# Performance work log

Measured on AMD Instinct MI355X. Metric: run time of the kernel, lower is better.

The kernel has to match this reference:

```python
import jax, jax.numpy as jnp
import numpy as np
from jax import lax

B, C_IN, L = 512, 32, 512
E = 8
POOL = 16            # AdaptiveAvgPool1d(16)
D_IN = C_IN * L      # expert input = flattened x
D_OUT = 768          # pooler_output dim (hard-coded in module)
TAU = 1.0            # gumbel temperature
BN_EPS = 1e-5


def setup_inputs() -> dict:
    key = jax.random.key(0)
    ks = jax.random.split(key, 8)
    s = 0.02
    return {
        "x": jax.random.normal(ks[0], (B, C_IN, L), jnp.float32),
        "gumbel_u": jax.random.uniform(ks[1], (B, E), jnp.float32, 1e-6, 1.0 - 1e-6),
        "conv_w": jax.random.normal(ks[2], (64, C_IN, 3), jnp.float32) * s,
        "conv_b": jnp.zeros((64,), jnp.float32),
        "bn_gamma": jnp.ones((64 * POOL,), jnp.float32),
        "bn_beta": jnp.zeros((64 * POOL,), jnp.float32),
        "bn_mean": jnp.zeros((64 * POOL,), jnp.float32),
        "bn_var": jnp.ones((64 * POOL,), jnp.float32),
        "fc1_w": jax.random.normal(ks[3], (128, 64 * POOL), jnp.float32) * s,
        "fc1_b": jnp.zeros((128,), jnp.float32),
        "fc2_w": jax.random.normal(ks[4], (E, 128), jnp.float32) * s,
        "fc2_b": jnp.zeros((E,), jnp.float32),
        "expert_w": jax.random.normal(ks[5], (E, D_IN, D_OUT), jnp.float32) * s,
        "expert_b": jnp.zeros((E, D_OUT), jnp.float32),
    }


def _gelu(v):
    return jax.nn.gelu(v, approximate=False)  # torch nn.GELU default (erf)


def reference(x, gumbel_u, conv_w, conv_b, bn_gamma, bn_beta, bn_mean, bn_var,
              fc1_w, fc1_b, fc2_w, fc2_b, expert_w, expert_b):
    # ---- router ----
    h = lax.conv_general_dilated(x, conv_w, (1,), ((1, 1),),
                                 dimension_numbers=("NCH", "OIH", "NCH"))
    h = _gelu(h + conv_b[None, :, None])                     # [B,64,L]
    h = h.reshape(B, 64, POOL, L // POOL).mean(-1)           # adaptive avg pool -> [B,64,16]
    h = h.reshape(B, 64 * POOL)                              # flatten
    h = (h - bn_mean) * lax.rsqrt(bn_var + BN_EPS) * bn_gamma + bn_beta  # BN (eval)
    h = _gelu(h @ fc1_w.T + fc1_b)                           # dropout inactive in eval
    logits = h @ fc2_w.T + fc2_b                             # [B,E]

    # ---- soft gumbel-softmax gating (hard=False), then top-2 ----
    g = -jnp.log(-jnp.log(gumbel_u))
    routing_weights = jax.nn.softmax((logits + g) / TAU, axis=1)
    topv, topi = lax.top_k(routing_weights, 2)               # [B,2]
    w = topv / (topv.sum(axis=1, keepdims=True) + 1e-8)      # [B,2]

    # ---- dispatch/compute/combine (dense-expert stand-in: flatten + linear) ----
    xf = x.reshape(B, D_IN)
    all_out = jnp.einsum("bd,edh->beh", xf, expert_w) + expert_b[None]  # [B,E,768]
    sel = jnp.take_along_axis(all_out, topi[:, :, None], axis=1)        # [B,2,768]
    pooler_output = (sel * w[:, :, None]).sum(axis=1)                   # [B,768]
    return pooler_output
```

## Files before the change

kernel.cpp:

```cpp
#include <hip/hip_runtime.h>
#include <hip/hip_bf16.h>

#define NB 512
#define CIN 32
#define LEN 512
#define NE 8
#define NPOOL 16
#define DIN 16384
#define DOUT 768
#define HD 1024
#define F1 128

#define MT 128
#define NT 128
#define BK 32

typedef __attribute__((ext_vector_type(4))) float f32x4;
typedef __attribute__((ext_vector_type(8))) short s16x8;
typedef __attribute__((ext_vector_type(4))) unsigned int u32x4;

__device__ __forceinline__ float gelu_erf(float v) {
    return 0.5f * v * (1.0f + erff(v * 0.70710678118654752f));
}

__device__ __forceinline__ unsigned cvt_pk(float lo, float hi) {
    unsigned r;
    asm volatile("v_cvt_pk_bf16_f32 %0, %1, %2" : "=v"(r) : "v"(lo), "v"(hi));
    return r;
}

__device__ __forceinline__ unsigned short f2bf_u(float f) {
    union { float f; unsigned u; } x; x.f = f;
    unsigned r = x.u + 0x7fffu + ((x.u >> 16) & 1u);
    return (unsigned short)(r >> 16);
}

__device__ __forceinline__ void gload_lds16(const void* gptr, void* lptr) {
    __builtin_amdgcn_global_load_lds(
        (const __attribute__((address_space(1))) unsigned int*)gptr,
        (__attribute__((address_space(3))) unsigned int*)lptr,
        16, 0, 0);
}

__device__ __forceinline__ int bswz(int kr) {
    int g3 = kr >> 3;
    return (g3 & 3) | ((g3 & 1) << 2);
}

__global__ __launch_bounds__(256) void krouter_conv(
    const float* __restrict__ x, const float* __restrict__ cw, const float* __restrict__ cb,
    const float* __restrict__ bng, const float* __restrict__ bnb,
    const float* __restrict__ bnm, const float* __restrict__ bnv,
    float* __restrict__ h, int* __restrict__ cnt)
{
    __shared__ float xs[CIN * 264];
    int half = blockIdx.x;
    int b = blockIdx.y;
    int t = threadIdx.x;
    if (b == 0 && half == 0 && t < NE) cnt[t] = 0;

    int Lchunk0 = half * 64 - 1;
    const float* xb = x + (size_t)b * DIN;
    for (int idx = t; idx < CIN * 66; idx += 256) {
        int ci = idx / 66;
        int cc = idx - ci * 66;
        int gc = min(max(Lchunk0 + cc, 0), 127);
        f32x4 v = *(const f32x4*)(xb + ci * 512 + gc * 4);
        int byte = ci * 1056 + ((cc << 4) ^ (((cc >> 3) & 7) << 4));
        *(f32x4*)((char*)xs + byte) = v;
    }
    __syncthreads();

    int p  = t & 7;
    int pg = half * 8 + p;
    int cq = t >> 3;
    int co0 = cq * 2, co1 = co0 + 1;

    float sa[32], sb[32];
    #pragma unroll
    for (int i = 0; i < 32; ++i) { sa[i] = 0.f; sb[i] = 0.f; }

    for (int ci = 0; ci < CIN; ++ci) {
        float f[40];
        #pragma unroll
        for (int u = 0; u < 10; ++u) {
            int lc = p * 8 + u;
            int byte = ci * 1056 + ((lc << 4) ^ (((lc >> 3) & 7) << 4));
            f32x4 v = *(const f32x4*)((const char*)xs + byte);
            f[4*u+0] = v[0]; f[4*u+1] = v[1]; f[4*u+2] = v[2]; f[4*u+3] = v[3];
        }
        if (pg == 0)  f[3]  = 0.f;
        if (pg == 15) f[36] = 0.f;
        float wa0 = cw[co0*96 + ci*3 + 0], wa1 = cw[co0*96 + ci*3 + 1], wa2 = cw[co0*96 + ci*3 + 2];
        float wb0 = cw[co1*96 + ci*3 + 0], wb1 = cw[co1*96 + ci*3 + 1], wb2 = cw[co1*96 + ci*3 + 2];
        #pragma unroll
        for (int i = 0; i < 32; ++i) {
            sa[i] = fmaf(f[i+3], wa0, fmaf(f[i+4], wa1, fmaf(f[i+5], wa2, sa[i])));
            sb[i] = fmaf(f[i+3], wb0, fmaf(f[i+4], wb1, fmaf(f[i+5], wb2, sb[i])));
        }
    }

    float ba = cb[co0], bbv = cb[co1];
    float ma = 0.f, mb = 0.f;
    #pragma unroll
    for (int i = 0; i < 32; ++i) { ma += gelu_erf(sa[i] + ba); mb += gelu_erf(sb[i] + bbv); }
    ma *= (1.f / 32.f); mb *= (1.f / 32.f);

    int oa = co0 * NPOOL + pg, ob = co1 * NPOOL + pg;
    float ra = (ma - bnm[oa]) * rsqrtf(bnv[oa] + 1e-5f) * bng[oa] + bnb[oa];
    float rb = (mb - bnm[ob]) * rsqrtf(bnv[ob] + 1e-5f) * bng[ob] + bnb[ob];
    h[(size_t)b * HD + oa] = ra;
    h[(size_t)b * HD + ob] = rb;
}

__global__ __launch_bounds__(256) void krouter_fc(
    const float* __restrict__ h, const float* __restrict__ f1w, const float* __restrict__ f1b,
    const float* __restrict__ f2w, const float* __restrict__ f2b,
    const float* __restrict__ gu,
    int* __restrict__ top2e, float* __restrict__ top2w,
    int* __restrict__ cnt, int* __restrict__ rowlist, float* __restrict__ roww)
{
    __shared__ float hs[8 * HD];
    __shared__ float h1s[8 * F1];
    __shared__ float lg[8 * NE];

    int bb = blockIdx.x * 8;
    int t = threadIdx.x;

    const f32x4* hg = (const f32x4*)(h + (size_t)bb * HD);
    f32x4* hs4 = (f32x4*)hs;
    #pragma unroll
    for (int u = 0; u < 8; ++u) hs4[t + 256 * u] = hg[t + 256 * u];
    __syncthreads();

    int j = t & 127;
    int pr = t >> 7;
    float acc[4] = {0.f, 0.f, 0.f, 0.f};
    const f32x4* w4 = (const f32x4*)(f1w + (size_t)j * HD);
    for (int k4 = 0; k4 < 256; ++k4) {
        f32x4 w = w4[k4];
        #pragma unroll
        for (int g = 0; g < 4; ++g) {
            f32x4 hv = hs4[(pr * 4 + g) * 256 + k4];
            acc[g] += w[0]*hv[0] + w[1]*hv[1] + w[2]*hv[2] + w[3]*hv[3];
        }
    }
    float bj = f1b[j];
    #pragma unroll
    for (int g = 0; g < 4; ++g) h1s[(pr * 4 + g) * F1 + j] = gelu_erf(acc[g] + bj);
    __syncthreads();

    if (t < 64) {
        int bi = t >> 3, e = t & 7;
        float s = f2b[e];
        const float* w = f2w + e * F1;
        const float* hh = h1s + bi * F1;
        #pragma unroll 8
        for (int k = 0; k < F1; ++k) s += hh[k] * w[k];
        lg[bi * NE + e] = s;
    }
    __syncthreads();

    if (t < 8) {
        int bi = t; int b = bb + bi;
        float r[NE];
        float mx = -1e30f;
        #pragma unroll
        for (int e = 0; e < NE; ++e) {
            float g = -logf(-logf(gu[b * NE + e]));
            r[e] = lg[bi * NE + e] + g;
            mx = fmaxf(mx, r[e]);
        }
        float sum = 0.f;
        #pragma unroll
        for (int e = 0; e < NE; ++e) { r[e] = expf(r[e] - mx); sum += r[e]; }
        float inv = 1.f / sum;
        #pragma unroll
        for (int e = 0; e < NE; ++e) r[e] *= inv;
        int e0 = 0; float v0 = r[0];
        #pragma unroll
        for (int e = 1; e < NE; ++e) if (r[e] > v0) { v0 = r[e]; e0 = e; }
        int e1 = -1; float v1 = -1.f;
        #pragma unroll
        for (int e = 0; e < NE; ++e) { if (e == e0) continue; if (r[e] > v1) { v1 = r[e]; e1 = e; } }
        float den = v0 + v1 + 1e-8f;
        float w0 = v0 / den, w1 = v1 / den;
        top2e[b * 2 + 0] = e0; top2e[b * 2 + 1] = e1;
        top2w[b * 2 + 0] = w0; top2w[b * 2 + 1] = w1;
        int p0 = atomicAdd(&cnt[e0], 1);
        rowlist[e0 * NB + p0] = b * 2 + 0; roww[e0 * NB + p0] = w0;
        int p1 = atomicAdd(&cnt[e1], 1);
        rowlist[e1 * NB + p1] = b * 2 + 1; roww[e1 * NB + p1] = w1;
    }
}

__global__ __launch_bounds__(512, 2) void kgemm(
    const float* __restrict__ x, const float* __restrict__ ew,
    const int* __restrict__ cnt, const int* __restrict__ rowlist, const float* __restrict__ roww,
    unsigned short* __restrict__ ypart, int nkc, int kch)
{
    int bid = blockIdx.x;
    int mt = bid & 1;
    int rest = bid >> 1;
    int kc = rest % nkc;
    int rest2 = rest / nkc;
    int nt = rest2 % 6;
    int e  = rest2 / 6;
    int cn = cnt[e];

    __shared__ __align__(16) char As[2][MT * BK * 2];
    __shared__ __align__(16) char Bs[2][BK * NT * 4];

    int t = threadIdx.x;
    int wid = t >> 6, lane = t & 63;
    int wm = wid >> 2, wn = wid & 3;
    int g = lane >> 4;
    int NS = kch / BK;
    int k0 = kc * kch;

    int seg0 = wid * 2, seg1 = wid * 2 + 1;
    const char* gB = (const char*)ew + (size_t)e * DIN * DOUT * 4
                   + (size_t)k0 * (DOUT * 4) + nt * NT * 4;
    int kr0 = seg0 * 2 + (lane >> 5), cs0 = lane & 31;
    int kr1 = seg1 * 2 + (lane >> 5), cs1 = lane & 31;
    const char* gp0 = gB + (size_t)kr0 * (DOUT * 4) + ((cs0 ^ bswz(kr0)) << 4);
    const char* gp1 = gB + (size_t)kr1 * (DOUT * 4) + ((cs1 ^ bswz(kr1)) << 4);

    int ar = t >> 2, aq = t & 3;
    int aoff = ar * 64 + (((aq ^ (ar & 3))) << 4);

    for (int row0 = mt * MT; row0 < cn; row0 += 2 * MT) {
        int mloc = min(MT, cn - row0);
        int arc = min(ar, mloc - 1);
        int ent_a = rowlist[e * NB + row0 + arc];
        const float* axp = x + (size_t)(ent_a >> 1) * DIN + k0 + aq * 8;
        bool wact = (wm * 64 < mloc);

        f32x4 acc[4][2];
        #pragma unroll
        for (int i = 0; i < 4; ++i)
            #pragma unroll
            for (int jj = 0; jj < 2; ++jj) acc[i][jj] = (f32x4){0.f, 0.f, 0.f, 0.f};

        f32x4 a0, a1;
        const char* bp0 = gp0;
        const char* bp1 = gp1;

        auto stageB = [&](int bi) {
            gload_lds16(bp0, (char*)Bs[bi] + seg0 * 1024);
            gload_lds16(bp1, (char*)Bs[bi] + seg1 * 1024);
        };
        auto loadA = [&](int s) {
            const f32x4* p = (const f32x4*)(axp + (size_t)s * BK);
            a0 = p[0]; a1 = p[1];
        };
        auto storeA = [&](int bi) {
            u32x4 pk;
            pk[0] = cvt_pk(a0[0], a0[1]); pk[1] = cvt_pk(a0[2], a0[3]);
            pk[2] = cvt_pk(a1[0], a1[1]); pk[3] = cvt_pk(a1[2], a1[3]);
            *(u32x4*)(As[bi] + aoff) = pk;
        };

        stageB(0);
        loadA(0);
        storeA(0);
        __syncthreads();

        for (int s = 0; s < NS; ++s) {
            int buf = s & 1;
            if (s + 1 < NS) {
                bp0 += BK * DOUT * 4;  bp1 += BK * DOUT * 4;
                stageB(buf ^ 1);
                loadA(s + 1);
            }

            if (wact) {
                const char* Ab = As[buf];
                const char* Bb = Bs[buf];
                s16x8 af[4];
                #pragma unroll
                for (int mi = 0; mi < 4; ++mi) {
                    int m = wm * 64 + mi * 16 + (lane & 15);
                    af[mi] = *(const s16x8*)(Ab + m * 64 + ((g ^ (m & 3)) << 4));
                }
                #pragma unroll
                for (int ni = 0; ni < 2; ++ni) {
                    int n = wn * 32 + ni * 16 + (lane & 15);
                    int sw = bswz(g * 8);
                    int cbase = (((n >> 2) ^ sw) << 4) + ((n & 3) << 2);
                    float v[8];
                    #pragma unroll
                    for (int j = 0; j < 8; ++j)
                        v[j] = *(const float*)(Bb + (g * 8 + j) * 512 + cbase);
                    union { u32x4 u; s16x8 s; } bf;
                    bf.u[0] = cvt_pk(v[0], v[1]); bf.u[1] = cvt_pk(v[2], v[3]);
                    bf.u[2] = cvt_pk(v[4], v[5]); bf.u[3] = cvt_pk(v[6], v[7]);
                    #pragma unroll
                    for (int mi = 0; mi < 4; ++mi)
                        acc[mi][ni] = __builtin_amdgcn_mfma_f32_16x16x32_bf16(af[mi], bf.s, acc[mi][ni], 0, 0, 0);
                }
            }

            if (s + 1 < NS) storeA(buf ^ 1);
            __syncthreads();
        }

        if (wact) {
            #pragma unroll
            for (int mi = 0; mi < 4; ++mi) {
                #pragma unroll
                for (int rg = 0; rg < 4; ++rg) {
                    int m = wm * 64 + mi * 16 + g * 4 + rg;
                    if (m < mloc) {
                        int ent = rowlist[e * NB + row0 + m];
                        float wgt = roww[e * NB + row0 + m];
                        int ob = ent >> 1, slot = ent & 1;
                        unsigned short* dst = ypart + ((size_t)(slot * nkc + kc) * NB + ob) * DOUT
                                            + nt * NT + wn * 32 + (lane & 15);
                        #pragma unroll
                        for (int ni = 0; ni < 2; ++ni)
                            dst[ni * 16] = f2bf_u(acc[mi][ni][rg] * wgt);
                    }
                }
            }
        }
        __syncthreads();
    }
}

__global__ __launch_bounds__(256) void kcombine(
    const unsigned short* __restrict__ ypart,
    const int* __restrict__ top2e, const float* __restrict__ top2w,
    const float* __restrict__ eb, float* __restrict__ out, int nplanes)
{
    int b = blockIdx.y;
    int n = blockIdx.x * 256 + threadIdx.x;
    float s = 0.f;
    for (int p = 0; p < nplanes; ++p) {
        unsigned v = ypart[((size_t)p * NB + b) * DOUT + n];
        union { unsigned u; float f; } c; c.u = v << 16;
        s += c.f;
    }
    int e0 = top2e[b * 2], e1 = top2e[b * 2 + 1];
    float w0 = top2w[b * 2], w1 = top2w[b * 2 + 1];
    s += w0 * eb[e0 * DOUT + n] + w1 * eb[e1 * DOUT + n];
    out[(size_t)b * DOUT + n] = s;
}

extern "C" void kernel_launch(void* const* d_in, const int* in_sizes, int n_in,
                              void* d_out, int out_size, void* d_ws, size_t ws_size,
                              hipStream_t stream)
{
    const float* x   = (const float*)d_in[0];
    const float* gu  = (const float*)d_in[1];
    const float* cw  = (const float*)d_in[2];
    const float* cb  = (const float*)d_in[3];
    const float* bng = (const float*)d_in[4];
    const float* bnb = (const float*)d_in[5];
    const float* bnm = (const float*)d_in[6];
    const float* bnv = (const float*)d_in[7];
    const float* f1w = (const float*)d_in[8];
    const float* f1b = (const float*)d_in[9];
    const float* f2w = (const float*)d_in[10];
    const float* f2b = (const float*)d_in[11];
    const float* ew  = (const float*)d_in[12];
    const float* eb  = (const float*)d_in[13];

    int nkc = (ws_size >= (size_t)40 * 1024 * 1024) ? 16 : 8;
    int kch = DIN / nkc;

    char* ws = (char*)d_ws;
    size_t off = 0;
    float* h       = (float*)(ws + off); off += (size_t)NB * HD * 4;
    int*   top2e   = (int*)(ws + off);   off += (size_t)NB * 2 * 4;
    float* top2w   = (float*)(ws + off); off += (size_t)NB * 2 * 4;
    int*   cnt     = (int*)(ws + off);   off += 256;
    int*   rowlist = (int*)(ws + off);   off += (size_t)NE * NB * 4;
    float* roww    = (float*)(ws + off); off += (size_t)NE * NB * 4;
    unsigned short* ypart = (unsigned short*)(ws + off);
    off += (size_t)2 * nkc * NB * DOUT * 2;

    krouter_conv<<<dim3(2, NB), 256, 0, stream>>>(x, cw, cb, bng, bnb, bnm, bnv, h, cnt);
    krouter_fc<<<NB / 8, 256, 0, stream>>>(h, f1w, f1b, f2w, f2b, gu,
                                           top2e, top2w, cnt, rowlist, roww);
    kgemm<<<NE * 6 * nkc * 2, 512, 0, stream>>>(x, ew, cnt, rowlist, roww, ypart, nkc, kch);
    kcombine<<<dim3(3, NB), 256, 0, stream>>>(ypart, top2e, top2w, eb, (float*)d_out, 2 * nkc);
}
```

Measured before the change: 276.6 us.

## Retile expert GEMM to 256x96 tiles with XCD-aware block remap

Changes the expert GEMM tile from 128x128 to 256x96 so that a single workgroup covers up to 256 routed rows. Each weight tile is then streamed from HBM once per workgroup, instead of once for each of the two M-tile workgroups. It also remaps block IDs so consecutive blocks land on the same XCD, and moves the A store earlier so one barrier per stage can be dropped. The cost is fewer total workgroups, a larger LDS A buffer, more accumulators per wave, and an uneven B-staging split across waves.

```diff
diff --git a/kernel.cpp b/kernel.cpp
--- a/kernel.cpp
+++ b/kernel.cpp
@@ -11,8 +11,8 @@
 #define HD 1024
 #define F1 128
 
-#define MT 128
-#define NT 128
+#define MT 256
+#define NT 96
 #define BK 32
 
 typedef __attribute__((ext_vector_type(4))) float f32x4;
@@ -42,9 +42,12 @@
         16, 0, 0);
 }
 
-__device__ __forceinline__ int bswz(int kr) {
-    int g3 = kr >> 3;
+__device__ __forceinline__ int bswz(int k) {
+    int g3 = k >> 3;
     return (g3 & 3) | ((g3 & 1) << 2);
+}
+__device__ __forceinline__ int akey(int m) {
+    return (m & 3) ^ ((m >> 2) & 3);
 }
 
 __global__ __launch_bounds__(256) void krouter_conv(
@@ -199,13 +202,12 @@
     const int* __restrict__ cnt, const int* __restrict__ rowlist, const float* __restrict__ roww,
     unsigned short* __restrict__ ypart, int nkc, int kch)
 {
-    int bid = blockIdx.x;
-    int mt = bid & 1;
-    int rest = bid >> 1;
-    int kc = rest % nkc;
-    int rest2 = rest / nkc;
-    int nt = rest2 % 6;
-    int e  = rest2 / 6;
+    int nwg = gridDim.x;
+    int cpx = nwg >> 3;
+    int wg = (blockIdx.x & 7) * cpx + (blockIdx.x >> 3);
+    int nt = wg & 7;
+    int kc = (wg >> 3) % nkc;
+    int e  = wg / (8 * nkc);
     int cn = cnt[e];
 
     __shared__ __align__(16) char As[2][MT * BK * 2];
@@ -213,65 +215,82 @@
 
     int t = threadIdx.x;
     int wid = t >> 6, lane = t & 63;
-    int wm = wid >> 2, wn = wid & 3;
+    int wm = wid >> 1, wn = wid & 1;
     int g = lane >> 4;
     int NS = kch / BK;
     int k0 = kc * kch;
 
-    int seg0 = wid * 2, seg1 = wid * 2 + 1;
     const char* gB = (const char*)ew + (size_t)e * DIN * DOUT * 4
                    + (size_t)k0 * (DOUT * 4) + nt * NT * 4;
-    int kr0 = seg0 * 2 + (lane >> 5), cs0 = lane & 31;
-    int kr1 = seg1 * 2 + (lane >> 5), cs1 = lane & 31;
-    const char* gp0 = gB + (size_t)kr0 * (DOUT * 4) + ((cs0 ^ bswz(kr0)) << 4);
-    const char* gp1 = gB + (size_t)kr1 * (DOUT * 4) + ((cs1 ^ bswz(kr1)) << 4);
-
-    int ar = t >> 2, aq = t & 3;
-    int aoff = ar * 64 + (((aq ^ (ar & 3))) << 4);
-
-    for (int row0 = mt * MT; row0 < cn; row0 += 2 * MT) {
+    int seg0 = wid;
+    int seg1 = (wid < 4) ? (8 + wid) : -1;
+    int off0 = seg0 * 1024 + lane * 16;
+    int k_0 = off0 / 384, c_0 = (off0 - k_0 * 384) >> 4;
+    const char* gp0 = gB + (size_t)k_0 * (DOUT * 4) + ((c_0 ^ bswz(k_0)) << 4);
+    const char* gp1 = nullptr;
+    int ldsoff1 = 0;
+    if (seg1 >= 0) {
+        int off1 = seg1 * 1024 + lane * 16;
+        int k_1 = off1 / 384, c_1 = (off1 - k_1 * 384) >> 4;
+        gp1 = gB + (size_t)k_1 * (DOUT * 4) + ((c_1 ^ bswz(k_1)) << 4);
+        ldsoff1 = seg1 * 1024;
+    }
+    int ldsoff0 = seg0 * 1024;
+
+    int ar = t >> 1, ah = t & 1;
+    int arow_byte = ar * 64;
+    int ak = akey(ar);
+    int ac0 = ((2 * ah) ^ ak) << 4;
+    int ac1 = ((2 * ah + 1) ^ ak) << 4;
+
+    for (int row0 = 0; row0 < cn; row0 += MT) {
         int mloc = min(MT, cn - row0);
         int arc = min(ar, mloc - 1);
         int ent_a = rowlist[e * NB + row0 + arc];
-        const float* axp = x + (size_t)(ent_a >> 1) * DIN + k0 + aq * 8;
+        const float* axp = x + (size_t)(ent_a >> 1) * DIN + k0 + ah * 16;
         bool wact = (wm * 64 < mloc);
 
-        f32x4 acc[4][2];
+        f32x4 acc[4][3];
         #pragma unroll
         for (int i = 0; i < 4; ++i)
             #pragma unroll
-            for (int jj = 0; jj < 2; ++jj) acc[i][jj] = (f32x4){0.f, 0.f, 0.f, 0.f};
-
-        f32x4 a0, a1;
+            for (int jj = 0; jj < 3; ++jj) acc[i][jj] = (f32x4){0.f, 0.f, 0.f, 0.f};
+
+        f32x4 a0, a1, a2, a3;
         const char* bp0 = gp0;
         const char* bp1 = gp1;
 
-        auto stageB = [&](int bi) {
-            gload_lds16(bp0, (char*)Bs[bi] + seg0 * 1024);
-            gload_lds16(bp1, (char*)Bs[bi] + seg1 * 1024);
-        };
         auto loadA = [&](int s) {
             const f32x4* p = (const f32x4*)(axp + (size_t)s * BK);
-            a0 = p[0]; a1 = p[1];
+            a0 = p[0]; a1 = p[1]; a2 = p[2]; a3 = p[3];
+        };
+        auto stageB = [&](int bi) {
+            gload_lds16(bp0, (char*)Bs[bi] + ldsoff0);
+            if (seg1 >= 0) gload_lds16(bp1, (char*)Bs[bi] + ldsoff1);
         };
         auto storeA = [&](int bi) {
-            u32x4 pk;
-            pk[0] = cvt_pk(a0[0], a0[1]); pk[1] = cvt_pk(a0[2], a0[3]);
-            pk[2] = cvt_pk(a1[0], a1[1]); pk[3] = cvt_pk(a1[2], a1[3]);
-            *(u32x4*)(As[bi] + aoff) = pk;
+            u32x4 pk0, pk1;
+            pk0[0] = cvt_pk(a0[0], a0[1]); pk0[1] = cvt_pk(a0[2], a0[3]);
+            pk0[2] = cvt_pk(a1[0], a1[1]); pk0[3] = cvt_pk(a1[2], a1[3]);
+            pk1[0] = cvt_pk(a2[0], a2[1]); pk1[1] = cvt_pk(a2[2], a2[3]);
+            pk1[2] = cvt_pk(a3[0], a3[1]); pk1[3] = cvt_pk(a3[2], a3[3]);
+            *(u32x4*)(As[bi] + arow_byte + ac0) = pk0;
+            *(u32x4*)(As[bi] + arow_byte + ac1) = pk1;
         };
 
+        loadA(0);
         stageB(0);
-        loadA(0);
         storeA(0);
         __syncthreads();
 
         for (int s = 0; s < NS; ++s) {
             int buf = s & 1;
             if (s + 1 < NS) {
-                bp0 += BK * DOUT * 4;  bp1 += BK * DOUT * 4;
+                loadA(s + 1);
+                bp0 += BK * DOUT * 4;
+                if (seg1 >= 0) bp1 += BK * DOUT * 4;
                 stageB(buf ^ 1);
-                loadA(s + 1);
+                storeA(buf ^ 1);
             }
 
             if (wact) {
@@ -281,17 +300,17 @@
                 #pragma unroll
                 for (int mi = 0; mi < 4; ++mi) {
                     int m = wm * 64 + mi * 16 + (lane & 15);
-                    af[mi] = *(const s16x8*)(Ab + m * 64 + ((g ^ (m & 3)) << 4));
+                    af[mi] = *(const s16x8*)(Ab + m * 64 + ((g ^ akey(m)) << 4));
                 }
+                int key = bswz(g * 8);
                 #pragma unroll
-                for (int ni = 0; ni < 2; ++ni) {
-                    int n = wn * 32 + ni * 16 + (lane & 15);
-                    int sw = bswz(g * 8);
-                    int cbase = (((n >> 2) ^ sw) << 4) + ((n & 3) << 2);
+                for (int ni = 0; ni < 3; ++ni) {
+                    int n = wn * 48 + ni * 16 + (lane & 15);
+                    int cbase = (((n >> 2) ^ key) << 4) + ((n & 3) << 2);
                     float v[8];
                     #pragma unroll
                     for (int j = 0; j < 8; ++j)
-                        v[j] = *(const float*)(Bb + (g * 8 + j) * 512 + cbase);
+                        v[j] = *(const float*)(Bb + (g * 8 + j) * 384 + cbase);
                     union { u32x4 u; s16x8 s; } bf;
                     bf.u[0] = cvt_pk(v[0], v[1]); bf.u[1] = cvt_pk(v[2], v[3]);
                     bf.u[2] = cvt_pk(v[4], v[5]); bf.u[3] = cvt_pk(v[6], v[7]);
@@ -300,8 +319,6 @@
                         acc[mi][ni] = __builtin_amdgcn_mfma_f32_16x16x32_bf16(af[mi], bf.s, acc[mi][ni], 0, 0, 0);
                 }
             }
-
-            if (s + 1 < NS) storeA(buf ^ 1);
             __syncthreads();
         }
 
@@ -316,15 +333,14 @@
                         float wgt = roww[e * NB + row0 + m];
                         int ob = ent >> 1, slot = ent & 1;
                         unsigned short* dst = ypart + ((size_t)(slot * nkc + kc) * NB + ob) * DOUT
-                                            + nt * NT + wn * 32 + (lane & 15);
+                                            + nt * NT + wn * 48 + (lane & 15);
                         #pragma unroll
-                        for (int ni = 0; ni < 2; ++ni)
+                        for (int ni = 0; ni < 3; ++ni)
                             dst[ni * 16] = f2bf_u(acc[mi][ni][rg] * wgt);
                     }
                 }
             }
         }
-        __syncthreads();
     }
 }
 
@@ -383,6 +399,6 @@
     krouter_conv<<<dim3(2, NB), 256, 0, stream>>>(x, cw, cb, bng, bnb, bnm, bnv, h, cnt);
     krouter_fc<<<NB / 8, 256, 0, stream>>>(h, f1w, f1b, f2w, f2b, gu,
                                            top2e, top2w, cnt, rowlist, roww);
-    kgemm<<<NE * 6 * nkc * 2, 512, 0, stream>>>(x, ew, cnt, rowlist, roww, ypart, nkc, kch);
+    kgemm<<<NE * nkc * 8, 512, 0, stream>>>(x, ew, cnt, rowlist, roww, ypart, nkc, kch);
     kcombine<<<dim3(3, NB), 256, 0, stream>>>(ypart, top2e, top2w, eb, (float*)d_out, 2 * nkc);
 }
```

After: 237.9 us. 14.0% less time.

## Pre-convert activations to bf16 and retile expert GEMM to 256x64 with XCD-aware mapping

Applied to the files above, without the earlier changes.

Adds a separate kernel that converts x to bf16 once, so the grouped expert GEMM loads half the A bytes and no longer repeats the conversion in every tile. The GEMM tile changes from 128x128 to 256x64, so each expert's gathered rows are covered by one M tile and the mt split goes away. The B staging layout and swizzle are reworked to match. Workgroup IDs are remapped across the 8 XCDs, and a sched_barrier is placed before the A store. The trade-offs are an extra pass over x (16 MB read, 8 MB written), a larger workspace that may change the nkc choice, and weaker reuse of B across rows when an expert has more than 256 rows.

```diff
diff --git a/kernel.cpp b/kernel.cpp
--- a/kernel.cpp
+++ b/kernel.cpp
@@ -11,8 +11,8 @@
 #define HD 1024
 #define F1 128
 
-#define MT 128
-#define NT 128
+#define MT 256
+#define NT 64
 #define BK 32
 
 typedef __attribute__((ext_vector_type(4))) float f32x4;
@@ -42,9 +42,16 @@
         16, 0, 0);
 }
 
-__device__ __forceinline__ int bswz(int kr) {
-    int g3 = kr >> 3;
-    return (g3 & 3) | ((g3 & 1) << 2);
+__global__ __launch_bounds__(256) void kcvt(const float* __restrict__ x,
+                                            unsigned short* __restrict__ xb)
+{
+    int i = blockIdx.x * 256 + threadIdx.x;
+    const f32x4* src = (const f32x4*)(x + (size_t)i * 8);
+    f32x4 v0 = src[0], v1 = src[1];
+    u32x4 pk;
+    pk[0] = cvt_pk(v0[0], v0[1]); pk[1] = cvt_pk(v0[2], v0[3]);
+    pk[2] = cvt_pk(v1[0], v1[1]); pk[3] = cvt_pk(v1[2], v1[3]);
+    *(u32x4*)(xb + (size_t)i * 8) = pk;
 }
 
 __global__ __launch_bounds__(256) void krouter_conv(
@@ -60,12 +67,12 @@
     if (b == 0 && half == 0 && t < NE) cnt[t] = 0;
 
     int Lchunk0 = half * 64 - 1;
-    const float* xb = x + (size_t)b * DIN;
+    const float* xb_ = x + (size_t)b * DIN;
     for (int idx = t; idx < CIN * 66; idx += 256) {
         int ci = idx / 66;
         int cc = idx - ci * 66;
         int gc = min(max(Lchunk0 + cc, 0), 127);
-        f32x4 v = *(const f32x4*)(xb + ci * 512 + gc * 4);
+        f32x4 v = *(const f32x4*)(xb_ + ci * 512 + gc * 4);
         int byte = ci * 1056 + ((cc << 4) ^ (((cc >> 3) & 7) << 4));
         *(f32x4*)((char*)xs + byte) = v;
     }
@@ -195,17 +202,16 @@
 }
 
 __global__ __launch_bounds__(512, 2) void kgemm(
-    const float* __restrict__ x, const float* __restrict__ ew,
+    const unsigned short* __restrict__ xb, const float* __restrict__ ew,
     const int* __restrict__ cnt, const int* __restrict__ rowlist, const float* __restrict__ roww,
     unsigned short* __restrict__ ypart, int nkc, int kch)
 {
-    int bid = blockIdx.x;
-    int mt = bid & 1;
-    int rest = bid >> 1;
-    int kc = rest % nkc;
-    int rest2 = rest / nkc;
-    int nt = rest2 % 6;
-    int e  = rest2 / 6;
+    int nwg = gridDim.x;
+    int cpx = nwg >> 3;
+    int wg = (blockIdx.x & 7) * cpx + (blockIdx.x >> 3);
+    int nt = wg % 12;
+    int kc = (wg / 12) % nkc;
+    int e  = wg / (12 * nkc);
     int cn = cnt[e];
 
     __shared__ __align__(16) char As[2][MT * BK * 2];
@@ -213,27 +219,31 @@
 
     int t = threadIdx.x;
     int wid = t >> 6, lane = t & 63;
-    int wm = wid >> 2, wn = wid & 3;
+    int wm = wid >> 1, wn = wid & 1;
     int g = lane >> 4;
     int NS = kch / BK;
     int k0 = kc * kch;
 
-    int seg0 = wid * 2, seg1 = wid * 2 + 1;
     const char* gB = (const char*)ew + (size_t)e * DIN * DOUT * 4
                    + (size_t)k0 * (DOUT * 4) + nt * NT * 4;
-    int kr0 = seg0 * 2 + (lane >> 5), cs0 = lane & 31;
-    int kr1 = seg1 * 2 + (lane >> 5), cs1 = lane & 31;
-    const char* gp0 = gB + (size_t)kr0 * (DOUT * 4) + ((cs0 ^ bswz(kr0)) << 4);
-    const char* gp1 = gB + (size_t)kr1 * (DOUT * 4) + ((cs1 ^ bswz(kr1)) << 4);
-
-    int ar = t >> 2, aq = t & 3;
-    int aoff = ar * 64 + (((aq ^ (ar & 3))) << 4);
-
-    for (int row0 = mt * MT; row0 < cn; row0 += 2 * MT) {
+    int bk_ = wid * 4 + (lane >> 4);
+    int bc_ = lane & 15;
+    int bkey = ((bk_ >> 3) & 3) << 2;
+    const char* gp = gB + (size_t)bk_ * (DOUT * 4) + ((bc_ ^ bkey) << 4);
+    int ldsB = wid * 1024;
+
+    int ar = t >> 1, ah = t & 1;
+    int akey_ = (ar >> 1) & 3;
+    int ach0 = ((2 * ah) ^ akey_) << 4;
+    int ach1 = ((2 * ah + 1) ^ akey_) << 4;
+
+    for (int row0 = 0; row0 < cn; row0 += MT) {
         int mloc = min(MT, cn - row0);
         int arc = min(ar, mloc - 1);
         int ent_a = rowlist[e * NB + row0 + arc];
-        const float* axp = x + (size_t)(ent_a >> 1) * DIN + k0 + aq * 8;
+        const char* axp = (const char*)xb
+                        + ((size_t)(ent_a >> 1) * DIN + k0) * 2 + ah * 32;
+        bool ado = (ar < mloc);
         bool wact = (wm * 64 < mloc);
 
         f32x4 acc[4][2];
@@ -242,36 +252,36 @@
             #pragma unroll
             for (int jj = 0; jj < 2; ++jj) acc[i][jj] = (f32x4){0.f, 0.f, 0.f, 0.f};
 
-        f32x4 a0, a1;
-        const char* bp0 = gp0;
-        const char* bp1 = gp1;
-
+        u32x4 A0, A1;
+        const char* bp = gp;
+
+        auto loadA = [&](int s) {
+            if (ado) {
+                const u32x4* p = (const u32x4*)(axp + (size_t)s * (BK * 2));
+                A0 = p[0]; A1 = p[1];
+            }
+        };
         auto stageB = [&](int bi) {
-            gload_lds16(bp0, (char*)Bs[bi] + seg0 * 1024);
-            gload_lds16(bp1, (char*)Bs[bi] + seg1 * 1024);
-        };
-        auto loadA = [&](int s) {
-            const f32x4* p = (const f32x4*)(axp + (size_t)s * BK);
-            a0 = p[0]; a1 = p[1];
+            gload_lds16(bp, (char*)Bs[bi] + ldsB);
         };
         auto storeA = [&](int bi) {
-            u32x4 pk;
-            pk[0] = cvt_pk(a0[0], a0[1]); pk[1] = cvt_pk(a0[2], a0[3]);
-            pk[2] = cvt_pk(a1[0], a1[1]); pk[3] = cvt_pk(a1[2], a1[3]);
-            *(u32x4*)(As[bi] + aoff) = pk;
+            if (ado) {
+                *(u32x4*)(As[bi] + ar * 64 + ach0) = A0;
+                *(u32x4*)(As[bi] + ar * 64 + ach1) = A1;
+            }
         };
 
+        loadA(0);
         stageB(0);
-        loadA(0);
         storeA(0);
         __syncthreads();
 
         for (int s = 0; s < NS; ++s) {
             int buf = s & 1;
             if (s + 1 < NS) {
-                bp0 += BK * DOUT * 4;  bp1 += BK * DOUT * 4;
+                loadA(s + 1);
+                bp += (size_t)BK * DOUT * 4;
                 stageB(buf ^ 1);
-                loadA(s + 1);
             }
 
             if (wact) {
@@ -281,17 +291,16 @@
                 #pragma unroll
                 for (int mi = 0; mi < 4; ++mi) {
                     int m = wm * 64 + mi * 16 + (lane & 15);
-                    af[mi] = *(const s16x8*)(Ab + m * 64 + ((g ^ (m & 3)) << 4));
+                    af[mi] = *(const s16x8*)(Ab + m * 64 + ((g ^ ((m >> 1) & 3)) << 4));
                 }
                 #pragma unroll
                 for (int ni = 0; ni < 2; ++ni) {
                     int n = wn * 32 + ni * 16 + (lane & 15);
-                    int sw = bswz(g * 8);
-                    int cbase = (((n >> 2) ^ sw) << 4) + ((n & 3) << 2);
+                    int cb = (((n >> 2) ^ (g << 2)) << 4) + ((n & 3) << 2);
                     float v[8];
                     #pragma unroll
                     for (int j = 0; j < 8; ++j)
-                        v[j] = *(const float*)(Bb + (g * 8 + j) * 512 + cbase);
+                        v[j] = *(const float*)(Bb + (g * 8 + j) * 256 + cb);
                     union { u32x4 u; s16x8 s; } bf;
                     bf.u[0] = cvt_pk(v[0], v[1]); bf.u[1] = cvt_pk(v[2], v[3]);
                     bf.u[2] = cvt_pk(v[4], v[5]); bf.u[3] = cvt_pk(v[6], v[7]);
@@ -301,6 +310,7 @@
                 }
             }
 
+            __builtin_amdgcn_sched_barrier(0);
             if (s + 1 < NS) storeA(buf ^ 1);
             __syncthreads();
         }
@@ -366,7 +376,7 @@
     const float* ew  = (const float*)d_in[12];
     const float* eb  = (const float*)d_in[13];
 
-    int nkc = (ws_size >= (size_t)40 * 1024 * 1024) ? 16 : 8;
+    int nkc = (ws_size >= (size_t)64 * 1024 * 1024) ? 16 : 8;
     int kch = DIN / nkc;
 
     char* ws = (char*)d_ws;
@@ -377,12 +387,15 @@
     int*   cnt     = (int*)(ws + off);   off += 256;
     int*   rowlist = (int*)(ws + off);   off += (size_t)NE * NB * 4;
     float* roww    = (float*)(ws + off); off += (size_t)NE * NB * 4;
+    unsigned short* xbuf = (unsigned short*)(ws + off);
+    off += (size_t)NB * DIN * 2;
     unsigned short* ypart = (unsigned short*)(ws + off);
     off += (size_t)2 * nkc * NB * DOUT * 2;
 
+    kcvt<<<(NB * DIN / 8 + 255) / 256, 256, 0, stream>>>(x, xbuf);
     krouter_conv<<<dim3(2, NB), 256, 0, stream>>>(x, cw, cb, bng, bnb, bnm, bnv, h, cnt);
     krouter_fc<<<NB / 8, 256, 0, stream>>>(h, f1w, f1b, f2w, f2b, gu,
                                            top2e, top2w, cnt, rowlist, roww);
-    kgemm<<<NE * 6 * nkc * 2, 512, 0, stream>>>(x, ew, cnt, rowlist, roww, ypart, nkc, kch);
+    kgemm<<<NE * nkc * 12, 512, 0, stream>>>(xbuf, ew, cnt, rowlist, roww, ypart, nkc, kch);
     kcombine<<<dim3(3, NB), 256, 0, stream>>>(ypart, top2e, top2w, eb, (float*)d_out, 2 * nkc);
 }
```

Result: faster. 263.2 us (-4.9%).
